# Kernel optimization log

Measured on AMD Instinct MI355X. Metric: run time of the kernel, lower is better.

The kernel has to match this reference:

```python
import jax, jax.numpy as jnp
from jax import lax
import numpy as np

B, T, D, H, L, O = 64, 256, 256, 256, 50, 2


def setup_inputs() -> dict:
    key = jax.random.key(0)
    ks = jax.random.split(key, 7)
    s = 0.05  # small init to keep gates out of saturation
    return {
        "x": jax.random.normal(ks[0], (B, T, D), jnp.float32),
        "W_ih": jax.random.normal(ks[1], (L, 4 * H, H), jnp.float32) * s,
        "W_hh": jax.random.normal(ks[2], (L, 4 * H, H), jnp.float32) * s,
        "b_ih": jax.random.normal(ks[3], (L, 4 * H), jnp.float32) * s,
        "b_hh": jax.random.normal(ks[4], (L, 4 * H), jnp.float32) * s,
        "W_out": jax.random.normal(ks[5], (O, H), jnp.float32) * s,
        "b_out": jax.random.normal(ks[6], (O,), jnp.float32) * s,
    }


def _lstm_layer(x_seq, wih, whh, bih, bhh):
    # x_seq: [B, T, H_in]; PyTorch gate order i, f, g, o
    b = x_seq.shape[0]
    h = wih.shape[0] // 4
    bias = bih + bhh
    # precompute input projections for all timesteps (one big GEMM)
    xg = jnp.einsum("bti,gi->btg", x_seq, wih) + bias  # [B, T, 4H]

    def step(carry, xg_t):
        hprev, cprev = carry
        gates = xg_t + hprev @ whh.T  # [B, 4H]
        i, f, g, o = jnp.split(gates, 4, axis=-1)
        i = jax.nn.sigmoid(i)
        f = jax.nn.sigmoid(f)
        g = jnp.tanh(g)
        o = jax.nn.sigmoid(o)
        c = f * cprev + i * g
        hnew = o * jnp.tanh(c)
        return (hnew, c), hnew

    h0 = jnp.zeros((b, h), x_seq.dtype)
    (_, _), hs = lax.scan(step, (h0, h0), jnp.swapaxes(xg, 0, 1))
    return jnp.swapaxes(hs, 0, 1)  # [B, T, H]


def reference(x, W_ih, W_hh, b_ih, b_hh, W_out, b_out):
    def layer_step(carry, p):
        wih, whh, bih, bhh = p
        return _lstm_layer(carry, wih, whh, bih, bhh), None

    y, _ = lax.scan(layer_step, x, (W_ih, W_hh, b_ih, b_hh))
    logits = jnp.einsum("bth,oh->bto", y, W_out) + b_out
    return jax.nn.sigmoid(logits)
```

## Files before the change

kernel.cpp:

```cpp
#include <hip/hip_runtime.h>
#include <hip/hip_bf16.h>
#include <stdint.h>
#include <string.h>

#define NB   64
#define NT   256
#define NH   256
#define NL   50
#define NK   512
#define NG   1024

typedef __attribute__((ext_vector_type(8)))  short   short8;
typedef __attribute__((ext_vector_type(8)))  __bf16  bf16x8;
typedef __attribute__((ext_vector_type(4)))  float   float4v;
typedef __attribute__((ext_vector_type(4)))  int     int4v;

#define LOG2E_F    1.44269504088896340736f
#define TWOLOG2E_F 2.88539008177792681472f

__device__ __forceinline__ unsigned short f2bf(float f) {
  union { float f; uint32_t u; } v; v.f = f;
  uint32_t u = v.u;
  uint32_t r = (u + 0x7FFFu + ((u >> 16) & 1u)) >> 16;
  return (unsigned short)r;
}
__device__ __forceinline__ float bf2f(unsigned short s) {
  union { uint32_t u; float f; } v; v.u = ((uint32_t)s) << 16;
  return v.f;
}
__device__ __forceinline__ float sig2(float x) {
  float e = __builtin_amdgcn_exp2f(-x);
  return __builtin_amdgcn_rcpf(1.0f + e);
}
__device__ __forceinline__ float th2(float x) {
  float e = __builtin_amdgcn_exp2f(-x);
  return __builtin_fmaf(2.0f, __builtin_amdgcn_rcpf(1.0f + e), -1.0f);
}

__device__ __forceinline__ short8 ldg_sc1_b128(const unsigned short* p) {
  short8 r;
  asm volatile("global_load_dwordx4 %0, %1, off sc1" : "=v"(r) : "v"(p) : "memory");
  return r;
}
__device__ __forceinline__ void stg_sc1_b128(unsigned short* p, short8 v) {
  asm volatile("global_store_dwordx4 %0, %1, off sc1" :: "v"(p), "v"(v) : "memory");
}
__device__ __forceinline__ void wait_vm0() {
  asm volatile("s_waitcnt vmcnt(0)" ::: "memory");
}
__device__ __forceinline__ void wave_wait_all4(const int* p) {
  for (;;) {
    int4v f;
    asm volatile("global_load_dwordx4 %0, %1, off sc1\n\ts_waitcnt vmcnt(0)"
                 : "=v"(f) : "v"(p) : "memory");
    if ((f[0] & f[1] & f[2] & f[3]) != 0) break;
  }
}

#define OFF_WSWZ  0
#define OFF_BIAS  52428800
#define OFF_XBF   52633600
#define OFF_HRING 61022208
#define OFF_Y     67575808
#define OFF_PROD  75964416
#define OFF_CONS  76169216

__global__ void prep_w(const float* __restrict__ Wih, const float* __restrict__ Whh,
                       unsigned short* __restrict__ Wswz) {
  int idx = blockIdx.x * 256 + threadIdx.x;
  int j   = idx & 7;
  int lam = (idx >> 3) & 63;
  int kt  = (idx >> 9) & 15;
  int q   = (idx >> 13) & 3;
  int c   = (idx >> 15) & 15;
  int l   = idx >> 19;
  int k   = kt * 32 + (lam >> 4) * 8 + j;
  int g   = q * 256 + c * 16 + (lam & 15);
  float v = (k < 256) ? Wih[(l * NG + g) * 256 + k]
                      : Whh[(l * NG + g) * 256 + (k - 256)];
  v *= (q == 2) ? TWOLOG2E_F : LOG2E_F;
  Wswz[idx] = f2bf(v);
}

__global__ void prep_bias(const float* __restrict__ bih, const float* __restrict__ bhh,
                          float* __restrict__ Bias) {
  int idx = blockIdx.x * 256 + threadIdx.x;
  int col = idx & 15; int q = (idx >> 4) & 3; int c = (idx >> 6) & 15; int l = idx >> 10;
  int g = q * 256 + c * 16 + col;
  float v = bih[l * NG + g] + bhh[l * NG + g];
  v *= (q == 2) ? TWOLOG2E_F : LOG2E_F;
  Bias[idx] = v;
}

__global__ void prep_x(const float* __restrict__ x, unsigned short* __restrict__ Xbf) {
  int idx = blockIdx.x * 256 + threadIdx.x;
  int d = idx & 255; int t = (idx >> 8) & 255; int b = idx >> 16;
  Xbf[(t * NB + b) * 256 + d] = f2bf(x[idx]);
}

__global__ void zero_flags(int* __restrict__ p) {
  p[blockIdx.x * 256 + threadIdx.x] = 0;
}

#define RSTRIDE 81
#define HSTRIDE 264
__global__ __launch_bounds__(256, 1) void lstm_persistent(
    const unsigned short* __restrict__ Wswz,
    const float* __restrict__ Bias,
    const unsigned short* __restrict__ Xbf,
    unsigned short* __restrict__ Hring,
    unsigned short* __restrict__ Y,
    int* __restrict__ prod4,
    int* __restrict__ cons4) {
  int xcd = blockIdx.x & 7;
  int jj  = blockIdx.x >> 3;
  int l   = xcd * 7 + (jj >> 2);
  int w   = jj & 3;
  if (jj >= 28 || l >= NL) return;
  int tid = threadIdx.x;

  __shared__ unsigned short hc[64 * RSTRIDE * 8];
  __shared__ unsigned short hout[64 * HSTRIDE];
  __shared__ int cnt_fl;

  int wv   = tid >> 6;
  int ln   = tid & 63;
  int c    = w * 4 + wv;
  int colg = ln & 15;
  int quad = ln >> 4;
  bool pvside = (wv & 1);
  int  brb    = wv >> 1;

  if (tid == 0) cnt_fl = 0;

  bf16x8 wreg[64];
  {
    const unsigned short* wp = Wswz + (size_t)(l * 16 + c) * 32768 + ln * 8;
#pragma unroll
    for (int i = 0; i < 64; ++i)
      wreg[i] = *(const bf16x8*)(wp + i * 512);
  }
  float bv[4];
  {
    const float* bp = Bias + l * NG + c * 64;
#pragma unroll
    for (int q = 0; q < 4; ++q) bv[q] = bp[q * 16 + colg];
  }

  float cr[4][4] = {};
  int j = c * 16 + colg;
  bool last = (l == NL - 1);

  for (int t = 0; t < NT; ++t) {
    {
      short8 v[16];
      int e  = ln & 31;
      int rs = ln >> 5;
      if (!pvside) {
        if (l > 0) wave_wait_all4(&prod4[((l - 1) * NT + t) * 4]);
        const unsigned short* In = (l == 0)
            ? (Xbf + t * (NB * 256))
            : (Hring + (((t & 3) * NL + (l - 1)) * NB) * 256);
#pragma unroll
        for (int i = 0; i < 16; ++i) {
          int b = i * 4 + brb * 2 + rs;
          v[i] = ldg_sc1_b128(In + b * 256 + e * 8);
        }
      } else if (t > 0) {
        wave_wait_all4(&prod4[(l * NT + (t - 1)) * 4]);
        const unsigned short* Pv = Hring + ((((t - 1) & 3) * NL + l) * NB) * 256;
#pragma unroll
        for (int i = 0; i < 16; ++i) {
          int b = i * 4 + brb * 2 + rs;
          v[i] = ldg_sc1_b128(Pv + b * 256 + e * 8);
        }
      } else {
#pragma unroll
        for (int i = 0; i < 16; ++i) v[i] = short8{0, 0, 0, 0, 0, 0, 0, 0};
      }
      wait_vm0();
      int kb = (pvside ? 32 : 0) + e;
#pragma unroll
      for (int i = 0; i < 16; ++i) {
        int b = i * 4 + brb * 2 + rs;
        *(short8*)(hc + (b * RSTRIDE + kb) * 8) = v[i];
      }
    }
    __syncthreads();
    if (tid == 0 && l > 0)
      __hip_atomic_store(&cons4[((l - 1) * NT + t) * 4 + w], 1,
                         __ATOMIC_RELAXED, __HIP_MEMORY_SCOPE_AGENT);

    float4v acc[4][4];
#pragma unroll
    for (int q = 0; q < 4; ++q) {
      float4v f4 = {bv[q], bv[q], bv[q], bv[q]};
#pragma unroll
      for (int m = 0; m < 4; ++m) acc[m][q] = f4;
    }
#pragma unroll
    for (int kt = 0; kt < 16; ++kt) {
      bf16x8 a[4];
#pragma unroll
      for (int m = 0; m < 4; ++m)
        a[m] = *(const bf16x8*)(hc + ((m * 16 + colg) * RSTRIDE + kt * 4 + quad) * 8);
#pragma unroll
      for (int m = 0; m < 4; ++m)
#pragma unroll
        for (int q = 0; q < 4; ++q)
          acc[m][q] = __builtin_amdgcn_mfma_f32_16x16x32_bf16(a[m], wreg[q * 16 + kt], acc[m][q], 0, 0, 0);
    }

#pragma unroll
    for (int m = 0; m < 4; ++m) {
      float hv[4];
#pragma unroll
      for (int r = 0; r < 4; ++r) {
        float gi = sig2(acc[m][0][r]);
        float gf = sig2(acc[m][1][r]);
        float gg = th2(acc[m][2][r]);
        float go = sig2(acc[m][3][r]);
        float cn = gf * cr[m][r] + gi * gg;
        cr[m][r] = cn;
        hv[r] = go * th2(cn * TWOLOG2E_F);
      }
      uint32_t pk01, pk23;
      asm("v_cvt_pk_bf16_f32 %0, %1, %2" : "=v"(pk01) : "v"(hv[0]), "v"(hv[1]));
      asm("v_cvt_pk_bf16_f32 %0, %1, %2" : "=v"(pk23) : "v"(hv[2]), "v"(hv[3]));
      unsigned short* hp = hout + (m * 16 + quad * 4) * HSTRIDE + j;
      hp[0]           = (unsigned short)pk01;
      hp[HSTRIDE]     = (unsigned short)(pk01 >> 16);
      hp[2 * HSTRIDE] = (unsigned short)pk23;
      hp[3 * HSTRIDE] = (unsigned short)(pk23 >> 16);
    }
    if (wv == 0 && !last && t >= 4) wave_wait_all4(&cons4[(l * NT + (t - 4)) * 4]);
    __syncthreads();

    {
      unsigned short* Hout = Hring + (((t & 3) * NL + l) * NB) * 256;
      unsigned short* Yout = Y + (t * NB) * 256;
#pragma unroll
      for (int pass = 0; pass < 2; ++pass) {
        int u   = pass * 256 + tid;
        int b   = u >> 3;
        int e8  = u & 7;
        int col = w * 64 + e8 * 8;
        short8 hv = *(const short8*)(hout + b * HSTRIDE + col);
        stg_sc1_b128(Hout + b * 256 + col, hv);
        if (last) *(short8*)(Yout + b * 256 + col) = hv;
      }
    }
    wait_vm0();
    if (ln == 0) {
      int old = atomicAdd(&cnt_fl, 1);
      if (old == 4 * t + 3)
        __hip_atomic_store(&prod4[(l * NT + t) * 4 + w], 1,
                           __ATOMIC_RELAXED, __HIP_MEMORY_SCOPE_AGENT);
    }
  }
}

__global__ void final_proj(const unsigned short* __restrict__ Y,
                           const float* __restrict__ Wout,
                           const float* __restrict__ bout,
                           float* __restrict__ out) {
  int t = blockIdx.x;
  int tid = threadIdx.x;
  int b = tid >> 1, o = tid & 1;
  const unsigned short* yrow = Y + (t * NB + b) * 256;
  const float* wr = Wout + o * 256;
  float s = bout[o];
  for (int k0 = 0; k0 < 256; k0 += 8) {
    short8 yv = *(const short8*)(yrow + k0);
#pragma unroll
    for (int e = 0; e < 8; ++e)
      s += bf2f(((unsigned short*)&yv)[e]) * wr[k0 + e];
  }
  out[(b * NT + t) * 2 + o] = 1.0f / (1.0f + __expf(-s));
}

extern "C" void kernel_launch(void* const* d_in, const int* in_sizes, int n_in,
                              void* d_out, int out_size, void* d_ws, size_t ws_size,
                              hipStream_t stream) {
  (void)in_sizes; (void)n_in; (void)out_size; (void)ws_size;
  const float* x    = (const float*)d_in[0];
  const float* Wih  = (const float*)d_in[1];
  const float* Whh  = (const float*)d_in[2];
  const float* bih  = (const float*)d_in[3];
  const float* bhh  = (const float*)d_in[4];
  const float* Wout = (const float*)d_in[5];
  const float* bout = (const float*)d_in[6];
  float* out = (float*)d_out;

  char* ws = (char*)d_ws;
  unsigned short* Wswz  = (unsigned short*)(ws + OFF_WSWZ);
  float*          Bias  = (float*)(ws + OFF_BIAS);
  unsigned short* Xbf   = (unsigned short*)(ws + OFF_XBF);
  unsigned short* Hring = (unsigned short*)(ws + OFF_HRING);
  unsigned short* Y     = (unsigned short*)(ws + OFF_Y);
  int*            prod4 = (int*)(ws + OFF_PROD);
  int*            cons4 = (int*)(ws + OFF_CONS);

  prep_w    <<<102400, 256, 0, stream>>>(Wih, Whh, Wswz);
  prep_bias <<<200,    256, 0, stream>>>(bih, bhh, Bias);
  prep_x    <<<16384,  256, 0, stream>>>(x, Xbf);
  zero_flags<<<400,    256, 0, stream>>>(prod4);

  lstm_persistent<<<256, 256, 0, stream>>>(Wswz, Bias, Xbf, Hring, Y, prod4, cons4);

  final_proj<<<NT, 128, 0, stream>>>(Y, Wout, bout, out);
}
```

Baseline: 2.006 ms.

## Replace producer flags with poison-sentinel data polling in the hidden-state ring

Removes the per-step producer flag (prod4) and the LDS counter handshake. Consumers now poll the hidden-state ring directly until no element equals a NaN-pattern sentinel, and they re-poison slots two steps later. The consumer backpressure flag load is issued early so its latency hides under the GEMM, and the cons4 signal is deferred by two steps. The aim is to cut one flag round-trip and a vmcnt wait from the critical inter-layer pipeline. The scheme relies on 16-byte stores being seen atomically and on real data never matching the sentinel.

Result: slower. 2.117 ms (+5.6%).

```diff
diff --git a/kernel.cpp b/kernel.cpp
--- a/kernel.cpp
+++ b/kernel.cpp
@@ -17,6 +17,7 @@
 
 #define LOG2E_F    1.44269504088896340736f
 #define TWOLOG2E_F 2.88539008177792681472f
+#define POIS_I     ((int)0x7F807F80)
 
 __device__ __forceinline__ unsigned short f2bf(float f) {
   union { float f; uint32_t u; } v; v.f = f;
@@ -42,11 +43,21 @@
   asm volatile("global_load_dwordx4 %0, %1, off sc1" : "=v"(r) : "v"(p) : "memory");
   return r;
 }
+__device__ __forceinline__ int4v ldg_sc1_i4(const int* p) {
+  int4v r;
+  asm volatile("global_load_dwordx4 %0, %1, off sc1" : "=v"(r) : "v"(p) : "memory");
+  return r;
+}
 __device__ __forceinline__ void stg_sc1_b128(unsigned short* p, short8 v) {
   asm volatile("global_store_dwordx4 %0, %1, off sc1" :: "v"(p), "v"(v) : "memory");
 }
 __device__ __forceinline__ void wait_vm0() {
   asm volatile("s_waitcnt vmcnt(0)" ::: "memory");
+}
+__device__ __forceinline__ int nonpois(short8 s) {
+  union { short8 v; int4v d; } u; u.v = s;
+  return (u.d[0] != POIS_I) & (u.d[1] != POIS_I) &
+         (u.d[2] != POIS_I) & (u.d[3] != POIS_I);
 }
 __device__ __forceinline__ void wave_wait_all4(const int* p) {
   for (;;) {
@@ -62,7 +73,7 @@
 #define OFF_XBF   52633600
 #define OFF_HRING 61022208
 #define OFF_Y     67575808
-#define OFF_PROD  75964416
+#define OFF_SPARE 75964416
 #define OFF_CONS  76169216
 
 __global__ void prep_w(const float* __restrict__ Wih, const float* __restrict__ Whh,
@@ -102,6 +113,10 @@
   p[blockIdx.x * 256 + threadIdx.x] = 0;
 }
 
+__global__ void poison_hring(int* __restrict__ p) {
+  p[blockIdx.x * 256 + threadIdx.x] = POIS_I;
+}
+
 #define RSTRIDE 81
 #define HSTRIDE 264
 __global__ __launch_bounds__(256, 1) void lstm_persistent(
@@ -110,7 +125,6 @@
     const unsigned short* __restrict__ Xbf,
     unsigned short* __restrict__ Hring,
     unsigned short* __restrict__ Y,
-    int* __restrict__ prod4,
     int* __restrict__ cons4) {
   int xcd = blockIdx.x & 7;
   int jj  = blockIdx.x >> 3;
@@ -121,7 +135,6 @@
 
   __shared__ unsigned short hc[64 * RSTRIDE * 8];
   __shared__ unsigned short hout[64 * HSTRIDE];
-  __shared__ int cnt_fl;
 
   int wv   = tid >> 6;
   int ln   = tid & 63;
@@ -131,8 +144,6 @@
   bool pvside = (wv & 1);
   int  brb    = wv >> 1;
 
-  if (tid == 0) cnt_fl = 0;
-
   bf16x8 wreg[64];
   {
     const unsigned short* wp = Wswz + (size_t)(l * 16 + c) * 32768 + ln * 8;
@@ -150,35 +161,50 @@
   float cr[4][4] = {};
   int j = c * 16 + colg;
   bool last = (l == NL - 1);
+  int e  = ln & 31;
+  int rs = ln >> 5;
 
   for (int t = 0; t < NT; ++t) {
     {
       short8 v[16];
-      int e  = ln & 31;
-      int rs = ln >> 5;
+      const unsigned short* base = nullptr;
       if (!pvside) {
-        if (l > 0) wave_wait_all4(&prod4[((l - 1) * NT + t) * 4]);
-        const unsigned short* In = (l == 0)
-            ? (Xbf + t * (NB * 256))
-            : (Hring + (((t & 3) * NL + (l - 1)) * NB) * 256);
-#pragma unroll
-        for (int i = 0; i < 16; ++i) {
-          int b = i * 4 + brb * 2 + rs;
-          v[i] = ldg_sc1_b128(In + b * 256 + e * 8);
+        if (l == 0) {
+          const unsigned short* In = Xbf + t * (NB * 256);
+#pragma unroll
+          for (int i = 0; i < 16; ++i) {
+            int b = i * 4 + brb * 2 + rs;
+            v[i] = *(const short8*)(In + b * 256 + e * 8);
+          }
+        } else {
+          base = Hring + (((t & 3) * NL + (l - 1)) * NB) * 256;
         }
       } else if (t > 0) {
-        wave_wait_all4(&prod4[(l * NT + (t - 1)) * 4]);
-        const unsigned short* Pv = Hring + ((((t - 1) & 3) * NL + l) * NB) * 256;
-#pragma unroll
-        for (int i = 0; i < 16; ++i) {
-          int b = i * 4 + brb * 2 + rs;
-          v[i] = ldg_sc1_b128(Pv + b * 256 + e * 8);
+        base = Hring + ((((t - 1) & 3) * NL + l) * NB) * 256;
+      } else {
+#pragma unroll
+        for (int i = 0; i < 16; ++i) v[i] = short8{0, 0, 0, 0, 0, 0, 0, 0};
+      }
+      if (base) {
+        for (;;) {
+          int ok = 1;
+#pragma unroll
+          for (int i = 0; i < 16; ++i) {
+            int b = i * 4 + brb * 2 + rs;
+            v[i] = ldg_sc1_b128(base + b * 256 + e * 8);
+          }
+          wait_vm0();
+#pragma unroll
+          for (int i = 0; i < 16; ++i) ok &= nonpois(v[i]);
+          if (__all(ok)) break;
+          for (;;) {
+            asm volatile("s_sleep 1");
+            short8 c0 = ldg_sc1_b128(base + (brb * 2 + rs) * 256 + e * 8);
+            wait_vm0();
+            if (__all(nonpois(c0))) break;
+          }
         }
-      } else {
-#pragma unroll
-        for (int i = 0; i < 16; ++i) v[i] = short8{0, 0, 0, 0, 0, 0, 0, 0};
-      }
-      wait_vm0();
+      }
       int kb = (pvside ? 32 : 0) + e;
 #pragma unroll
       for (int i = 0; i < 16; ++i) {
@@ -187,9 +213,27 @@
       }
     }
     __syncthreads();
-    if (tid == 0 && l > 0)
-      __hip_atomic_store(&cons4[((l - 1) * NT + t) * 4 + w], 1,
-                         __ATOMIC_RELAXED, __HIP_MEMORY_SCOPE_AGENT);
+
+    if (t >= 2) {
+      unsigned short* pbase = nullptr;
+      if (!pvside && l > 0)
+        pbase = Hring + ((((t - 2) & 3) * NL + (l - 1)) * NB) * 256;
+      else if (pvside && last)
+        pbase = Hring + ((((t - 2) & 3) * NL + l) * NB) * 256;
+      if (pbase && (e >> 3) == w) {
+        short8 pz;
+        { union { int4v d; short8 s; } u;
+          u.d = int4v{POIS_I, POIS_I, POIS_I, POIS_I}; pz = u.s; }
+#pragma unroll
+        for (int i = 0; i < 16; ++i) {
+          int b = i * 4 + brb * 2 + rs;
+          stg_sc1_b128(pbase + b * 256 + e * 8, pz);
+        }
+      }
+    }
+    bool ckbp = (wv == 0) && (t >= 4);
+    int4v cf = int4v{1, 1, 1, 1};
+    if (ckbp) cf = ldg_sc1_i4(&cons4[(l * NT + (t - 4)) * 4]);
 
     float4v acc[4][4];
 #pragma unroll
@@ -233,8 +277,18 @@
       hp[2 * HSTRIDE] = (unsigned short)pk23;
       hp[3 * HSTRIDE] = (unsigned short)(pk23 >> 16);
     }
-    if (wv == 0 && !last && t >= 4) wave_wait_all4(&cons4[(l * NT + (t - 4)) * 4]);
+    if (ckbp && !(cf[0] & cf[1] & cf[2] & cf[3]))
+      wave_wait_all4(&cons4[(l * NT + (t - 4)) * 4]);
     __syncthreads();
+
+    if (t >= 2) {
+      if (tid == 0 && l > 0)
+        __hip_atomic_store(&cons4[((l - 1) * NT + (t - 2)) * 4 + w], 1,
+                           __ATOMIC_RELAXED, __HIP_MEMORY_SCOPE_AGENT);
+      if (tid == 64 && last)
+        __hip_atomic_store(&cons4[(l * NT + (t - 2)) * 4 + w], 1,
+                           __ATOMIC_RELAXED, __HIP_MEMORY_SCOPE_AGENT);
+    }
 
     {
       unsigned short* Hout = Hring + (((t & 3) * NL + l) * NB) * 256;
@@ -249,13 +303,6 @@
         stg_sc1_b128(Hout + b * 256 + col, hv);
         if (last) *(short8*)(Yout + b * 256 + col) = hv;
       }
-    }
-    wait_vm0();
-    if (ln == 0) {
-      int old = atomicAdd(&cnt_fl, 1);
-      if (old == 4 * t + 3)
-        __hip_atomic_store(&prod4[(l * NT + t) * 4 + w], 1,
-                           __ATOMIC_RELAXED, __HIP_MEMORY_SCOPE_AGENT);
     }
   }
 }
@@ -298,15 +345,15 @@
   unsigned short* Xbf   = (unsigned short*)(ws + OFF_XBF);
   unsigned short* Hring = (unsigned short*)(ws + OFF_HRING);
   unsigned short* Y     = (unsigned short*)(ws + OFF_Y);
-  int*            prod4 = (int*)(ws + OFF_PROD);
   int*            cons4 = (int*)(ws + OFF_CONS);
 
-  prep_w    <<<102400, 256, 0, stream>>>(Wih, Whh, Wswz);
-  prep_bias <<<200,    256, 0, stream>>>(bih, bhh, Bias);
-  prep_x    <<<16384,  256, 0, stream>>>(x, Xbf);
-  zero_flags<<<400,    256, 0, stream>>>(prod4);
-
-  lstm_persistent<<<256, 256, 0, stream>>>(Wswz, Bias, Xbf, Hring, Y, prod4, cons4);
+  prep_w      <<<102400, 256, 0, stream>>>(Wih, Whh, Wswz);
+  prep_bias   <<<200,    256, 0, stream>>>(bih, bhh, Bias);
+  prep_x      <<<16384,  256, 0, stream>>>(x, Xbf);
+  zero_flags  <<<400,    256, 0, stream>>>((int*)(ws + OFF_SPARE));
+  poison_hring<<<6400,   256, 0, stream>>>((int*)(ws + OFF_HRING));
+
+  lstm_persistent<<<256, 256, 0, stream>>>(Wswz, Bias, Xbf, Hring, Y, cons4);
 
   final_proj<<<NT, 128, 0, stream>>>(Y, Wout, bout, out);
 }
```
